# Kernel tuning notes

Hardware: AMD Instinct MI355X
Metric: run time of the kernel (lower is better)

The kernel has to match this reference:

```python
import jax, jax.numpy as jnp
import numpy as np
import math
from jax import lax

B, L, D, P, V, K = 4, 2048, 512, 128, 8, 4


def _lin(x, w, b):
    # torch Linear: y = x @ W^T + b, W shape (out, in)
    return jnp.einsum('...i,oi->...o', x, w) + b


def _gelu(v):
    return jax.nn.gelu(v, approximate=False)


def _dwconv_causal(x_ncl, w, b):
    # depthwise causal conv: torch Conv1d(groups=D, padding=K-1) then [:, :, :L]
    y = lax.conv_general_dilated(x_ncl, w, (1,), [(K - 1, 0)],
                                 dimension_numbers=('NCH', 'OIH', 'NCH'),
                                 feature_group_count=D)
    return y + b[None, :, None]


def _ln(v, g, b):
    m = v.mean(-1, keepdims=True)
    var = v.var(-1, keepdims=True)
    return (v - m) / jnp.sqrt(var + 1e-5) * g + b


def setup_inputs() -> dict:
    key = jax.random.key(0)
    it = iter(jax.random.split(key, 64))
    def nrm(shape, s=0.02):
        return jax.random.normal(next(it), shape, dtype=jnp.float32) * s
    z = lambda *s: jnp.zeros(s, jnp.float32)
    return dict(
        x=nrm((B, L, D), 1.0),
        lc_w=nrm((D, 1, K)), lc_b=z(D),
        cg_w=nrm((D, 1, K)), cg_b=z(D),
        cp_w=nrm((D, D)), cp_b=z(D),
        tw_w=nrm((D, D)), tw_b=z(D),
        omega_scale=jnp.full((D,), 0.01, jnp.float32),
        pi0_w=nrm((D, D)), pi0_b=z(D),
        pi2_w=nrm((D, D)), pi2_b=z(D),
        m1v_w=nrm((D, D)), m1v_b=z(D),
        m1o_w=nrm((D, D)), m1o_b=z(D),
        mag_w=nrm((D, D)), mag_b=z(D),
        mag_scale=jnp.asarray(5.0, jnp.float32),
        qo_w=nrm((D, D)), qo_b=z(D),
        ke_w=nrm((P, D)), ke_b=z(P),
        ve_w=nrm((V, D)), ve_b=z(V),
        sk0_w=nrm((D, 2 * D)), sk0_b=z(D),
        sk2_w=nrm((P, D)), sk2_b=z(P),
        sg_w=nrm((1, D)), sg_b=z(1),
        kvo_w=nrm((D, V)), kvo_b=z(D),
        ln_g=jnp.ones(5 * D, jnp.float32), ln_b=z(5 * D),
        o1_w=nrm((2 * D, 5 * D)), o1_b=z(2 * D),
        o2_w=nrm((D, 2 * D)), o2_b=z(D),
    )


def reference(x, lc_w, lc_b, cg_w, cg_b, cp_w, cp_b, tw_w, tw_b, omega_scale,
              pi0_w, pi0_b, pi2_w, pi2_b, m1v_w, m1v_b, m1o_w, m1o_b,
              mag_w, mag_b, mag_scale, qo_w, qo_b, ke_w, ke_b, ve_w, ve_b,
              sk0_w, sk0_b, sk2_w, sk2_b, sg_w, sg_b, kvo_w, kvo_b,
              ln_g, ln_b, o1_w, o1_b, o2_w, o2_b):
    Bs, Ls, Ds = x.shape
    # local gated causal depthwise conv branch
    xc = jnp.transpose(x, (0, 2, 1))                          # (B, D, L)
    co = _dwconv_causal(xc, lc_w, lc_b)
    cg = jax.nn.sigmoid(_dwconv_causal(xc, cg_w, cg_b))
    conv_out = _lin(jnp.transpose(co * cg, (0, 2, 1)), cp_w, cp_b)
    # evolving phases
    omega_scaled = _lin(x, tw_w, tw_b) * jnp.abs(omega_scale)
    phi = _lin(_gelu(_lin(x, pi0_w, pi0_b)), pi2_w, pi2_b) + jnp.cumsum(omega_scaled, axis=1)
    cos_phi = jnp.cos(phi)
    sin_phi = jnp.sin(phi)
    # magnitude-weighted phase memory
    v1 = _lin(x, m1v_w, m1v_b)
    magnitude = jax.nn.sigmoid(_lin(x, mag_w, mag_b)) * jnp.abs(mag_scale)
    wv1 = magnitude * v1
    sqrt_mag = jnp.sqrt(jnp.cumsum(magnitude, axis=1) + 1e-8)
    mem1_cos = jnp.cumsum(wv1 * cos_phi, axis=1) / sqrt_mag
    mem1_sin = jnp.cumsum(wv1 * sin_phi, axis=1) / sqrt_mag
    phi_q = phi + _lin(x, qo_w, qo_b)
    pos_ret = (mem1_cos * jnp.cos(phi_q) + mem1_sin * jnp.sin(phi_q)) / math.sqrt(Ds)
    pos_out = _lin(pos_ret, m1o_w, m1o_b)
    # phase-keyed associative KV memory
    query_phase = jnp.tanh(_lin(x, ke_w, ke_b)) * math.pi    # (B, L, P)
    values = _lin(x, ve_w, ve_b)                              # (B, L, V)
    store_gate = jax.nn.sigmoid(_lin(x, sg_w, sg_b))          # (B, L, 1)
    positions = jnp.arange(1, Ls + 1, dtype=x.dtype).reshape(1, -1, 1)
    context_avg = jnp.cumsum(x, axis=1) / positions
    storage_phase = jnp.tanh(_lin(_gelu(_lin(jnp.concatenate([x, context_avg], -1), sk0_w, sk0_b)), sk2_w, sk2_b)) * math.pi
    gated_vals = values * store_gate                          # (B, L, V)
    kv_mem_cos = jnp.cumsum(jnp.cos(storage_phase)[..., None] * gated_vals[:, :, None, :], axis=1)
    kv_mem_sin = jnp.cumsum(jnp.sin(storage_phase)[..., None] * gated_vals[:, :, None, :], axis=1)
    gate_norm = jnp.sqrt(jnp.maximum(jnp.cumsum(store_gate, axis=1), 1.0))[..., None]  # (B, L, 1, 1)
    kv_mem_cos = kv_mem_cos / gate_norm
    kv_mem_sin = kv_mem_sin / gate_norm
    kv_retrieved = (jnp.cos(query_phase)[..., None] * kv_mem_cos +
                    jnp.sin(query_phase)[..., None] * kv_mem_sin).sum(axis=2) / math.sqrt(P)
    kv_out = _lin(kv_retrieved, kvo_w, kvo_b)
    # combine (dropout is identity in eval)
    combined = jnp.concatenate([conv_out, pos_out, kv_out, x * cos_phi, x * sin_phi], axis=-1)
    h = _ln(combined, ln_g, ln_b)
    h = _lin(_gelu(_lin(h, o1_w, o1_b)), o2_w, o2_b)
    return x + h
```

## Files before the change

kernel.cpp:

```cpp
#include <hip/hip_runtime.h>
#include <cstdint>

typedef unsigned short u16;
typedef short short8 __attribute__((ext_vector_type(8)));
typedef float floatx4 __attribute__((ext_vector_type(4)));

#define B_ 4
#define L_ 2048
#define D_ 512
#define P_ 128
#define V_ 8
#define BL (B_ * L_)
#define NC_ 128
#define CH_ 16
#define PI_F 3.14159265358979323846f

__device__ inline u16 f2b(float f) {
    unsigned u = __float_as_uint(f);
    unsigned r = u + 0x7FFFu + ((u >> 16) & 1u);
    return (u16)(r >> 16);
}
__device__ inline float b2f(u16 h) {
    return __uint_as_float(((unsigned)h) << 16);
}
__device__ inline float gelu_f(float v) {
    return 0.5f * v * (1.0f + erff(v * 0.70710678118654752f));
}
__device__ inline float sigm(float v) {
    return 1.0f / (1.0f + __expf(-v));
}
__device__ inline float tanh_fast(float v) {
    return 1.0f - 2.0f / (1.0f + __expf(2.0f * v));
}

__device__ inline void async16(const u16* g, u16* l) {
    __builtin_amdgcn_global_load_lds(
        (const __attribute__((address_space(1))) unsigned int*)g,
        (__attribute__((address_space(3))) unsigned int*)l, 16, 0, 0);
}

extern __shared__ u16 smem_dyn[];

enum { EPI_F32 = 0, EPI_BF16 = 1, EPI_GELU_BF16 = 2, EPI_RESID_F32 = 3,
       EPI_PASS1 = 4, EPI_ATOMIC = 5 };

template <int EPI>
__device__ __forceinline__ void gemm_body(
    const u16* __restrict__ A, int lda,
    const u16* __restrict__ W, int ldw,
    const float* __restrict__ bias,
    void* __restrict__ Cout, int ldc, int N, int K,
    const float* __restrict__ resid, int mt, int nt)
{
    const int tid  = threadIdx.x;
    const int lane = tid & 63;
    const int wid  = tid >> 6;
    const int wm   = wid & 1, wn = wid >> 1;
    const int l16  = lane & 15, quad = lane >> 4;

    floatx4 acc[4][4] = {};

    const u16* Ab = A + (size_t)(mt * 128) * lda;
    const u16* Wb = W + (size_t)(nt * 128) * ldw;

    const int srow = lane >> 2;
    const int scol = (lane & 3) * 8;
    const u16* ga0 = Ab + (size_t)(wid * 16 + srow) * lda + scol;
    const u16* ga1 = Ab + (size_t)(64 + wid * 16 + srow) * lda + scol;
    const u16* gb0 = Wb + (size_t)(wid * 16 + srow) * ldw + scol;
    const u16* gb1 = Wb + (size_t)(64 + wid * 16 + srow) * ldw + scol;

    const int lA0 = (wid * 16) * 32;
    const int lA1 = (64 + wid * 16) * 32;

    const int nsteps = K >> 5;

    auto stage = [&](int t, int s) {
        u16* base = smem_dyn + s * 8192;
        const int ko = t * 32;
        async16(ga0 + ko, base + lA0);
        async16(ga1 + ko, base + lA1);
        async16(gb0 + ko, base + 4096 + lA0);
        async16(gb1 + ko, base + 4096 + lA1);
    };

    stage(0, 0);
    if (nsteps > 1) stage(1, 1);

    int s = 0;
    for (int t = 0; t < nsteps; ++t) {
        if (t + 1 < nsteps) {
            asm volatile("s_waitcnt vmcnt(4)" ::: "memory");
        } else {
            asm volatile("s_waitcnt vmcnt(0)" ::: "memory");
        }
        __builtin_amdgcn_s_barrier();
        asm volatile("" ::: "memory");
        if (t + 2 < nsteps) {
            int s2 = s + 2; if (s2 >= 3) s2 -= 3;
            stage(t + 2, s2);
        }
        const u16* As = smem_dyn + s * 8192;
        const u16* Bs = As + 4096;
        short8 a[4], b[4];
#pragma unroll
        for (int i = 0; i < 4; i++)
            a[i] = *(const short8*)(&As[(wm * 64 + i * 16 + l16) * 32 + quad * 8]);
#pragma unroll
        for (int j = 0; j < 4; j++)
            b[j] = *(const short8*)(&Bs[(wn * 64 + j * 16 + l16) * 32 + quad * 8]);
        __builtin_amdgcn_s_setprio(1);
#pragma unroll
        for (int i = 0; i < 4; i++)
#pragma unroll
            for (int j = 0; j < 4; j++)
                acc[i][j] = __builtin_amdgcn_mfma_f32_16x16x32_bf16(a[i], b[j], acc[i][j], 0, 0, 0);
        __builtin_amdgcn_s_setprio(0);
        ++s; if (s >= 3) s -= 3;
    }

#pragma unroll
    for (int i = 0; i < 4; i++) {
#pragma unroll
        for (int j = 0; j < 4; j++) {
#pragma unroll
            for (int r = 0; r < 4; r++) {
                int grow = mt * 128 + wm * 64 + i * 16 + quad * 4 + r;
                int gcol = nt * 128 + wn * 64 + j * 16 + l16;
                if (gcol < N) {
                    float v = acc[i][j][r] + (bias ? bias[gcol] : 0.0f);
                    size_t off = (size_t)grow * ldc + gcol;
                    if (EPI == EPI_F32)            ((float*)Cout)[off] = v;
                    else if (EPI == EPI_BF16)      ((u16*)Cout)[off] = f2b(v);
                    else if (EPI == EPI_GELU_BF16) ((u16*)Cout)[off] = f2b(gelu_f(v));
                    else if (EPI == EPI_PASS1) {
                        float vv = (gcol >= 512 && gcol < 1024) ? gelu_f(v) : v;
                        ((u16*)Cout)[off] = f2b(vv);
                    }
                    else if (EPI == EPI_RESID_F32) ((float*)Cout)[off] = v + resid[off];
                    else                           atomicAdd(&((float*)Cout)[off], v);
                }
            }
        }
    }
}

template <int EPI>
__global__ __launch_bounds__(256)
void gemm256(const u16* __restrict__ A, int lda,
             const u16* __restrict__ W, int ldw,
             const float* __restrict__ bias,
             void* __restrict__ C, int ldc, int N, int K,
             const float* __restrict__ resid)
{
    int kz = blockIdx.z;
    gemm_body<EPI>(A + (size_t)kz * K, lda, W + (size_t)kz * K, ldw,
                   kz == 0 ? bias : nullptr, C, ldc, N, K, resid,
                   blockIdx.x, blockIdx.y);
}

__global__ __launch_bounds__(256)
void mega1(const u16* __restrict__ xcat, const u16* __restrict__ convg,
           const u16* __restrict__ wcat1, const float* __restrict__ bcat1,
           const u16* __restrict__ kesgw, const float* __restrict__ kesgb,
           const u16* __restrict__ cpw, const float* __restrict__ cp_b,
           u16* __restrict__ out1, float* __restrict__ kesgo, u16* __restrict__ combined)
{
    int y = blockIdx.y, mt = blockIdx.x;
    if (y < 20)
        gemm_body<EPI_PASS1>(xcat, 1024, wcat1, 512, bcat1, out1, 2560, 2560, 512, nullptr, mt, y);
    else if (y < 22)
        gemm_body<EPI_F32>(xcat, 1024, kesgw, 512, kesgb, kesgo, 144, 144, 512, nullptr, mt, y - 20);
    else
        gemm_body<EPI_BF16>(convg, 512, cpw, 512, cp_b, combined, 2560, 512, 512, nullptr, mt, y - 22);
}

__global__ __launch_bounds__(256)
void mega2(const u16* __restrict__ posret, const u16* __restrict__ xcat,
           const u16* __restrict__ m1ow, const float* __restrict__ m1o_b,
           const u16* __restrict__ sk0w, const float* __restrict__ sk0_b,
           u16* __restrict__ combined, u16* __restrict__ sk0g)
{
    int y = blockIdx.y, mt = blockIdx.x;
    if (y < 4)
        gemm_body<EPI_BF16>(posret, 512, m1ow, 512, m1o_b, combined + 512, 2560, 512, 512, nullptr, mt, y);
    else
        gemm_body<EPI_GELU_BF16>(xcat, 1024, sk0w, 1024, sk0_b, sk0g, 512, 512, 1024, nullptr, mt, y - 4);
}

__global__ __launch_bounds__(256)
void prep_weights(const float* tw, const float* pi0, const float* m1v, const float* mag, const float* qo,
                  const float* ke, const float* ve, const float* sg,
                  const float* pi2, const float* cp, const float* sk0, const float* sk2,
                  const float* m1o, const float* o1, const float* o2,
                  const float* tw_b, const float* pi0_b, const float* m1v_b, const float* mag_b, const float* qo_b,
                  const float* ke_b, const float* ve_b, const float* sg_b,
                  u16* wcat1, float* bcat1, u16* kesgw, float* kesgb,
                  u16* pi2w, u16* cpw, u16* sk0w, u16* sk2w, u16* m1ow, u16* o1w, u16* o2w)
{
    int idx = blockIdx.x * 256 + threadIdx.x;
    const int n0 = 2560 * 512;
    const int n1 = n0 + 256 * 512;
    const int n2 = n1 + 512 * 512;
    const int n3 = n2 + 512 * 512;
    const int n4 = n3 + 512 * 1024;
    const int n5 = n4 + 128 * 512;
    const int n6 = n5 + 512 * 512;
    const int n7 = n6 + 1024 * 2560;
    const int n8 = n7 + 512 * 1024;
    const int n9 = n8 + 2560;
    const int n10 = n9 + 256;
    if (idx < n0) {
        int r = idx >> 9, k = idx & 511;
        const float* s = (r < 512) ? tw : (r < 1024) ? pi0 : (r < 1536) ? m1v : (r < 2048) ? mag : qo;
        wcat1[idx] = f2b(s[(r & 511) * 512 + k]);
    } else if (idx < n1) {
        int i = idx - n0; int r = i >> 9, k = i & 511;
        float v;
        if (r < 128)      v = ke[r * 512 + k];
        else if (r < 136) v = ve[(r - 128) * 512 + k];
        else if (r == 136) v = sg[k];
        else               v = 0.0f;
        kesgw[i] = f2b(v);
    }
    else if (idx < n2) { int i = idx - n1; pi2w[i] = f2b(pi2[i]); }
    else if (idx < n3) { int i = idx - n2; cpw[i]  = f2b(cp[i]); }
    else if (idx < n4) { int i = idx - n3; sk0w[i] = f2b(sk0[i]); }
    else if (idx < n5) { int i = idx - n4; sk2w[i] = f2b(sk2[i]); }
    else if (idx < n6) { int i = idx - n5; m1ow[i] = f2b(m1o[i]); }
    else if (idx < n7) { int i = idx - n6; o1w[i]  = f2b(o1[i]); }
    else if (idx < n8) { int i = idx - n7; o2w[i]  = f2b(o2[i]); }
    else if (idx < n9) {
        int i = idx - n8;
        const float* s = (i < 512) ? tw_b : (i < 1024) ? pi0_b : (i < 1536) ? m1v_b : (i < 2048) ? mag_b : qo_b;
        bcat1[i] = s[i & 511];
    } else if (idx < n10) {
        int i = idx - n9;
        kesgb[i] = (i < 128) ? ke_b[i] : (i < 136) ? ve_b[i - 128] : (i == 136) ? sg_b[0] : 0.0f;
    }
}

__global__ __launch_bounds__(256)
void conv_gate(const float* __restrict__ x,
               const float* __restrict__ lcw, const float* __restrict__ lcb,
               const float* __restrict__ cgw, const float* __restrict__ cgb,
               u16* __restrict__ out, u16* __restrict__ xcat)
{
    int idx = blockIdx.x * 256 + threadIdx.x;
    int d = idx & 511; int bl = idx >> 9;
    int l = bl & (L_ - 1); int b = bl >> 11;
    float a0 = 0.f, a1 = 0.f, xv3 = 0.f;
#pragma unroll
    for (int k = 0; k < 4; k++) {
        int ls = l - 3 + k;
        if (ls >= 0) {
            float xv = x[((size_t)(b * L_ + ls)) * 512 + d];
            if (k == 3) xv3 = xv;
            a0 += xv * lcw[d * 4 + k];
            a1 += xv * cgw[d * 4 + k];
        }
    }
    a0 += lcb[d];
    a1 = sigm(a1 + cgb[d]);
    out[idx] = f2b(a0 * a1);
    xcat[(size_t)bl * 1024 + d] = f2b(xv3);
}

__device__ __forceinline__ void scan_a_body(
    int blk, const u16* __restrict__ out1, const float* __restrict__ x,
    const float* __restrict__ oscale, const float* __restrict__ msc,
    float* __restrict__ cs_o, float* __restrict__ cs_x, float* __restrict__ cs_m)
{
    int nc = blk & 15, dt = (blk >> 4) & 7, b = blk >> 7;
    int t = threadIdx.x; int dl = t & 63, lg = t >> 6;
    int d = dt * 64 + dl;
    float os = fabsf(oscale[d]);
    float ms = fabsf(msc[0]);
    float so = 0.f, sx = 0.f, sm = 0.f;
    int l0 = nc * 128 + lg * 32;
    for (int i = 0; i < 32; i++) {
        size_t r = (size_t)(b * L_ + l0 + i);
        so += b2f(out1[r * 2560 + d]) * os;
        sm += sigm(b2f(out1[r * 2560 + 1536 + d])) * ms;
        sx += x[r * 512 + d];
    }
    __shared__ float sh[3][4][64];
    sh[0][lg][dl] = so; sh[1][lg][dl] = sx; sh[2][lg][dl] = sm;
    __syncthreads();
    if (t < 64) {
        float a = 0.f, xx = 0.f, m = 0.f;
        for (int g = 0; g < 4; g++) { a += sh[0][g][t]; xx += sh[1][g][t]; m += sh[2][g][t]; }
        size_t o = ((size_t)(b * 16 + nc)) * 512 + dt * 64 + t;
        cs_o[o] = a; cs_x[o] = xx; cs_m[o] = m;
    }
}

__device__ __forceinline__ void gate_body(const float* __restrict__ kesgo,
                                          float* __restrict__ gni)
{
    int b = threadIdx.x >> 6; int lane = threadIdx.x & 63;
    float v[32]; float s = 0.f;
#pragma unroll
    for (int i = 0; i < 32; i++) {
        int l = lane * 32 + i;
        v[i] = sigm(kesgo[((size_t)(b * L_ + l)) * 144 + 136]);
        s += v[i];
    }
    float sc = s;
#pragma unroll
    for (int ofs = 1; ofs < 64; ofs <<= 1) {
        float t = __shfl_up(sc, ofs, 64);
        if (lane >= ofs) sc += t;
    }
    float run = sc - s;
#pragma unroll
    for (int i = 0; i < 32; i++) {
        run += v[i];
        gni[b * L_ + lane * 32 + i] = rsqrtf(fmaxf(run, 1.0f));
    }
}

__global__ __launch_bounds__(256)
void stage2(const u16* __restrict__ out1, const u16* __restrict__ pi2w,
            const float* __restrict__ pi2_b, u16* __restrict__ phib,
            const float* __restrict__ x, const float* __restrict__ oscale,
            const float* __restrict__ msc,
            float* __restrict__ cs_o, float* __restrict__ cs_x, float* __restrict__ cs_m,
            const float* __restrict__ kesgo, float* __restrict__ gni)
{
    int blk = blockIdx.x;
    if (blk < 256)
        gemm_body<EPI_BF16>(out1 + 512, 2560, pi2w, 512, pi2_b, phib, 512, 512, 512,
                            nullptr, blk & 63, blk >> 6);
    else if (blk < 768)
        scan_a_body(blk - 256, out1, x, oscale, msc, cs_o, cs_x, cs_m);
    else
        gate_body(kesgo, gni);
}

__global__ __launch_bounds__(256)
void scan_c(const u16* __restrict__ out1, const u16* __restrict__ phib,
            const float* __restrict__ oscale, const float* __restrict__ msc,
            const float* __restrict__ cs_o,
            float* __restrict__ phi, float* __restrict__ cs_wc, float* __restrict__ cs_ws)
{
    int blk = blockIdx.x;
    int nc = blk & 15, dt = (blk >> 4) & 7, b = blk >> 7;
    int t = threadIdx.x; int dl = t & 63, lg = t >> 6;
    int d = dt * 64 + dl;
    float os = fabsf(oscale[d]);
    float ms = fabsf(msc[0]);
    int l0 = nc * 128 + lg * 32;
    float so = 0.f;
    for (int i = 0; i < 32; i++) {
        size_t r = (size_t)(b * L_ + l0 + i);
        so += b2f(out1[r * 2560 + d]) * os;
    }
    __shared__ float sh[4][64];
    __shared__ float shw[2][4][64];
    sh[lg][dl] = so;
    __syncthreads();
    float pre = 0.f;
    for (int p = 0; p < nc; p++) pre += cs_o[((size_t)(b * 16 + p)) * 512 + d];
    for (int g = 0; g < lg; g++) pre += sh[g][dl];
    float cum = pre, swc = 0.f, sws = 0.f;
    for (int i = 0; i < 32; i++) {
        size_t r = (size_t)(b * L_ + l0 + i);
        cum += b2f(out1[r * 2560 + d]) * os;
        float ph = b2f(phib[r * 512 + d]) + cum;
        phi[r * 512 + d] = ph;
        float mg = sigm(b2f(out1[r * 2560 + 1536 + d])) * ms;
        float wv = mg * b2f(out1[r * 2560 + 1024 + d]);
        float s = __sinf(ph), c = __cosf(ph);
        swc += wv * c; sws += wv * s;
    }
    shw[0][lg][dl] = swc; shw[1][lg][dl] = sws;
    __syncthreads();
    if (t < 64) {
        float a = 0.f, bb = 0.f;
        for (int g = 0; g < 4; g++) { a += shw[0][g][t]; bb += shw[1][g][t]; }
        size_t o = ((size_t)(b * 16 + nc)) * 512 + dt * 64 + t;
        cs_wc[o] = a; cs_ws[o] = bb;
    }
}

__global__ __launch_bounds__(256)
void scan_e(const u16* __restrict__ out1, const float* __restrict__ phi,
            const float* __restrict__ x, const float* __restrict__ msc,
            const float* __restrict__ cs_m, const float* __restrict__ cs_x,
            const float* __restrict__ cs_wc, const float* __restrict__ cs_ws,
            u16* __restrict__ posret, u16* __restrict__ xcat, u16* __restrict__ combined)
{
    int blk = blockIdx.x;
    int nc = blk & 15, dt = (blk >> 4) & 7, b = blk >> 7;
    int t = threadIdx.x; int dl = t & 63, lg = t >> 6;
    int d = dt * 64 + dl;
    float ms = fabsf(msc[0]);
    int l0 = nc * 128 + lg * 32;
    float sm = 0.f, swc = 0.f, sws = 0.f, sx = 0.f;
    for (int i = 0; i < 32; i++) {
        size_t r = (size_t)(b * L_ + l0 + i);
        float ph = phi[r * 512 + d];
        float mg = sigm(b2f(out1[r * 2560 + 1536 + d])) * ms;
        float wv = mg * b2f(out1[r * 2560 + 1024 + d]);
        float s = __sinf(ph), c = __cosf(ph);
        sm += mg; swc += wv * c; sws += wv * s; sx += x[r * 512 + d];
    }
    __shared__ float sh[4][4][64];
    sh[0][lg][dl] = sm; sh[1][lg][dl] = swc; sh[2][lg][dl] = sws; sh[3][lg][dl] = sx;
    __syncthreads();
    float cm = 0.f, cwc = 0.f, cws = 0.f, cx = 0.f;
    for (int p = 0; p < nc; p++) {
        size_t o = ((size_t)(b * 16 + p)) * 512 + d;
        cm += cs_m[o]; cwc += cs_wc[o]; cws += cs_ws[o]; cx += cs_x[o];
    }
    for (int g = 0; g < lg; g++) {
        cm += sh[0][g][dl]; cwc += sh[1][g][dl]; cws += sh[2][g][dl]; cx += sh[3][g][dl];
    }
    const float invsqD = 0.044194173824159216f;
    for (int i = 0; i < 32; i++) {
        int l = l0 + i;
        size_t r = (size_t)(b * L_ + l);
        float ph = phi[r * 512 + d];
        float mg = sigm(b2f(out1[r * 2560 + 1536 + d])) * ms;
        float wv = mg * b2f(out1[r * 2560 + 1024 + d]);
        float xv = x[r * 512 + d];
        float s = __sinf(ph), c = __cosf(ph);
        cm += mg; cwc += wv * c; cws += wv * s; cx += xv;
        float smag = sqrtf(cm + 1e-8f);
        float m1c = cwc / smag, m1s = cws / smag;
        float phq = ph + b2f(out1[r * 2560 + 2048 + d]);
        float sq = __sinf(phq), cq = __cosf(phq);
        float pr = (m1c * cq + m1s * sq) * invsqD;
        posret[r * 512 + d] = f2b(pr);
        xcat[r * 1024 + 512 + d] = f2b(cx / (float)(l + 1));
        combined[r * 2560 + 1536 + d] = f2b(xv * c);
        combined[r * 2560 + 2048 + d] = f2b(xv * s);
    }
}

__global__ __launch_bounds__(64)
void kv_chunk(const float* __restrict__ sppre, const float* __restrict__ kesgo,
              float* __restrict__ spc, float* __restrict__ sps,
              float* __restrict__ csum)
{
    int blk = blockIdx.x; int nc = blk & (NC_ - 1), b = blk >> 7;
    int t = threadIdx.x;
    float Sc[2][8] = {}, Ss[2][8] = {};
    for (int i = 0; i < CH_; i++) {
        size_t r = (size_t)(b * L_ + nc * CH_ + i);
        float sgate = sigm(kesgo[r * 144 + 136]);
        float g[8];
#pragma unroll
        for (int v = 0; v < 8; v++) g[v] = kesgo[r * 144 + 128 + v] * sgate;
#pragma unroll
        for (int j = 0; j < 2; j++) {
            int p = t + j * 64;
            float sp = tanh_fast(sppre[r * 128 + p]) * PI_F;
            float s = __sinf(sp), c = __cosf(sp);
            spc[r * 128 + p] = c; sps[r * 128 + p] = s;
#pragma unroll
            for (int v = 0; v < 8; v++) { Sc[j][v] += c * g[v]; Ss[j][v] += s * g[v]; }
        }
    }
    size_t base = (size_t)blk * 2048;
#pragma unroll
    for (int j = 0; j < 2; j++)
#pragma unroll
        for (int v = 0; v < 8; v++) {
            csum[base + (t + j * 64) * 8 + v]        = Sc[j][v];
            csum[base + 1024 + (t + j * 64) * 8 + v] = Ss[j][v];
        }
}

__global__ __launch_bounds__(256)
void kv_scan(const float* __restrict__ cin, float* __restrict__ cex)
{
    int t = blockIdx.x * 256 + threadIdx.x;
    int pv = t & 1023; int cs = (t >> 10) & 1; int b = t >> 11;
    float run = 0.f;
    for (int nc = 0; nc < NC_; nc++) {
        size_t o = ((size_t)(b * NC_ + nc)) * 2048 + cs * 1024 + pv;
        cex[o] = run; run += cin[o];
    }
}

__global__ __launch_bounds__(64)
void kv_retrieve(const float* __restrict__ spc, const float* __restrict__ sps,
                 const float* __restrict__ kesgo,
                 const float* __restrict__ gni, const float* __restrict__ cex,
                 const float* __restrict__ kvo_w, const float* __restrict__ kvo_b,
                 u16* __restrict__ combined)
{
    int blk = blockIdx.x; int nc = blk & (NC_ - 1), b = blk >> 7;
    int t = threadIdx.x;
    const int nb = t * 8;
    float wr[8][8], br[8];
#pragma unroll
    for (int n = 0; n < 8; n++) {
        *(float4*)&wr[n][0] = *(const float4*)&kvo_w[(nb + n) * 8];
        *(float4*)&wr[n][4] = *(const float4*)&kvo_w[(nb + n) * 8 + 4];
        br[n] = kvo_b[nb + n];
    }
    float Sc[2][8], Ss[2][8];
    size_t base = (size_t)blk * 2048;
#pragma unroll
    for (int j = 0; j < 2; j++)
#pragma unroll
        for (int v = 0; v < 8; v++) {
            Sc[j][v] = cex[base + (t + j * 64) * 8 + v];
            Ss[j][v] = cex[base + 1024 + (t + j * 64) * 8 + v];
        }
    for (int i = 0; i < CH_; i++) {
        size_t r = (size_t)(b * L_ + nc * CH_ + i);
        float sgate = sigm(kesgo[r * 144 + 136]);
        float g[8];
#pragma unroll
        for (int v = 0; v < 8; v++) g[v] = kesgo[r * 144 + 128 + v] * sgate;
        float part[8];
#pragma unroll
        for (int v = 0; v < 8; v++) part[v] = 0.f;
#pragma unroll
        for (int j = 0; j < 2; j++) {
            int p = t + j * 64;
            float c = spc[r * 128 + p], s = sps[r * 128 + p];
#pragma unroll
            for (int v = 0; v < 8; v++) { Sc[j][v] += c * g[v]; Ss[j][v] += s * g[v]; }
            float qp = tanh_fast(kesgo[r * 144 + p]) * PI_F;
            float sq = __sinf(qp), cq = __cosf(qp);
#pragma unroll
            for (int v = 0; v < 8; v++) part[v] += cq * Sc[j][v] + sq * Ss[j][v];
        }
#pragma unroll
        for (int ofs = 1; ofs < 64; ofs <<= 1)
#pragma unroll
            for (int v = 0; v < 8; v++) part[v] += __shfl_xor(part[v], ofs, 64);
        float scale = gni[r] * 0.08838834764831845f;
        float pv[8];
#pragma unroll
        for (int v = 0; v < 8; v++) pv[v] = part[v] * scale;
        u16 outv[8];
#pragma unroll
        for (int n = 0; n < 8; n++) {
            float a = br[n];
#pragma unroll
            for (int v = 0; v < 8; v++) a += pv[v] * wr[n][v];
            outv[n] = f2b(a);
        }
        *(uint4*)&combined[r * 2560 + 1024 + nb] = *(const uint4*)outv;
    }
}

__global__ __launch_bounds__(320)
void ln_rows(u16* __restrict__ combined, const float* __restrict__ g, const float* __restrict__ bb)
{
    size_t m = blockIdx.x; int t = threadIdx.x;
    u16 vv[8];
    *(uint4*)vv = *(const uint4*)&combined[m * 2560 + t * 8];
    float f[8]; float s = 0.f, s2 = 0.f;
#pragma unroll
    for (int k = 0; k < 8; k++) { f[k] = b2f(vv[k]); s += f[k]; s2 += f[k] * f[k]; }
#pragma unroll
    for (int ofs = 1; ofs < 64; ofs <<= 1) {
        s  += __shfl_xor(s, ofs, 64);
        s2 += __shfl_xor(s2, ofs, 64);
    }
    __shared__ float shs[5], shs2[5];
    int wv = t >> 6;
    if ((t & 63) == 0) { shs[wv] = s; shs2[wv] = s2; }
    __syncthreads();
    float S = 0.f, S2 = 0.f;
#pragma unroll
    for (int i = 0; i < 5; i++) { S += shs[i]; S2 += shs2[i]; }
    float mean = S * (1.0f / 2560.0f);
    float var  = S2 * (1.0f / 2560.0f) - mean * mean;
    float rstd = rsqrtf(var + 1e-5f);
#pragma unroll
    for (int k = 0; k < 8; k++) {
        int c = t * 8 + k;
        vv[k] = f2b((f[k] - mean) * rstd * g[c] + bb[c]);
    }
    *(uint4*)&combined[m * 2560 + t * 8] = *(const uint4*)vv;
}

extern "C" void kernel_launch(void* const* d_in, const int* in_sizes, int n_in,
                              void* d_out, int out_size, void* d_ws, size_t ws_size,
                              hipStream_t stream)
{
    const float* x     = (const float*)d_in[0];
    const float* lc_w  = (const float*)d_in[1];
    const float* lc_b  = (const float*)d_in[2];
    const float* cg_w  = (const float*)d_in[3];
    const float* cg_b  = (const float*)d_in[4];
    const float* cp_w  = (const float*)d_in[5];
    const float* cp_b  = (const float*)d_in[6];
    const float* tw_w  = (const float*)d_in[7];
    const float* tw_b  = (const float*)d_in[8];
    const float* omega_scale = (const float*)d_in[9];
    const float* pi0_w = (const float*)d_in[10];
    const float* pi0_b = (const float*)d_in[11];
    const float* pi2_w = (const float*)d_in[12];
    const float* pi2_b = (const float*)d_in[13];
    const float* m1v_w = (const float*)d_in[14];
    const float* m1v_b = (const float*)d_in[15];
    const float* m1o_w = (const float*)d_in[16];
    const float* m1o_b = (const float*)d_in[17];
    const float* mag_w = (const float*)d_in[18];
    const float* mag_b = (const float*)d_in[19];
    const float* mag_scale = (const float*)d_in[20];
    const float* qo_w  = (const float*)d_in[21];
    const float* qo_b  = (const float*)d_in[22];
    const float* ke_w  = (const float*)d_in[23];
    const float* ke_b  = (const float*)d_in[24];
    const float* ve_w  = (const float*)d_in[25];
    const float* ve_b  = (const float*)d_in[26];
    const float* sk0_w = (const float*)d_in[27];
    const float* sk0_b = (const float*)d_in[28];
    const float* sk2_w = (const float*)d_in[29];
    const float* sk2_b = (const float*)d_in[30];
    const float* sg_w  = (const float*)d_in[31];
    const float* sg_b  = (const float*)d_in[32];
    const float* kvo_w = (const float*)d_in[33];
    const float* kvo_b = (const float*)d_in[34];
    const float* ln_g  = (const float*)d_in[35];
    const float* ln_b  = (const float*)d_in[36];
    const float* o1_w  = (const float*)d_in[37];
    const float* o1_b  = (const float*)d_in[38];
    const float* o2_w  = (const float*)d_in[39];
    const float* o2_b  = (const float*)d_in[40];
    float* out = (float*)d_out;

    char* base = (char*)d_ws;
    size_t off = 0;
    auto alloc = [&](size_t bytes) -> void* {
        void* p = base + off;
        off += (bytes + 255) & ~(size_t)255;
        return p;
    };

    u16*   wcat1  = (u16*)  alloc((size_t)2560 * 512 * 2);
    float* bcat1  = (float*)alloc(2560 * 4);
    u16*   kesgw  = (u16*)  alloc((size_t)256 * 512 * 2);
    float* kesgb  = (float*)alloc(256 * 4);
    u16*   pi2w   = (u16*)  alloc((size_t)512 * 512 * 2);
    u16*   cpw    = (u16*)  alloc((size_t)512 * 512 * 2);
    u16*   sk0w   = (u16*)  alloc((size_t)512 * 1024 * 2);
    u16*   sk2w   = (u16*)  alloc((size_t)128 * 512 * 2);
    u16*   m1ow   = (u16*)  alloc((size_t)512 * 512 * 2);
    u16*   o1w    = (u16*)  alloc((size_t)1024 * 2560 * 2);
    u16*   o2w    = (u16*)  alloc((size_t)512 * 1024 * 2);
    u16*   xcat   = (u16*)  alloc((size_t)BL * 1024 * 2);
    u16*   out1   = (u16*)  alloc((size_t)BL * 2560 * 2);
    u16*   phib   = (u16*)  alloc((size_t)BL * 512 * 2);
    float* phi    = (float*)alloc((size_t)BL * 512 * 4);
    float* kesgo  = (float*)alloc((size_t)BL * 144 * 4);
    u16*   convg  = (u16*)  alloc((size_t)BL * 512 * 2);
    float* sppre  = (float*)alloc((size_t)BL * 128 * 4);
    u16*   combined = (u16*)alloc((size_t)BL * 2560 * 2);
    float* cs_o   = (float*)alloc((size_t)4 * 16 * 512 * 4);
    float* cs_x   = (float*)alloc((size_t)4 * 16 * 512 * 4);
    float* cs_m   = (float*)alloc((size_t)4 * 16 * 512 * 4);
    float* cs_wc  = (float*)alloc((size_t)4 * 16 * 512 * 4);
    float* cs_ws  = (float*)alloc((size_t)4 * 16 * 512 * 4);
    float* gni    = (float*)alloc((size_t)BL * 4);
    u16*   posret = convg;
    u16*   sk0g   = out1;
    float* spc    = phi;
    float* sps    = phi + (size_t)BL * 128;
    float* kvcs   = (float*)phib;
    float* kvex   = (float*)phib + (size_t)B_ * NC_ * 2048;
    u16*   o1g    = xcat;
    (void)ws_size; (void)in_sizes; (void)n_in; (void)out_size;

    const size_t SMEM = 49152;

    prep_weights<<<23307, 256, 0, stream>>>(
        tw_w, pi0_w, m1v_w, mag_w, qo_w, ke_w, ve_w, sg_w,
        pi2_w, cp_w, sk0_w, sk2_w, m1o_w, o1_w, o2_w,
        tw_b, pi0_b, m1v_b, mag_b, qo_b, ke_b, ve_b, sg_b,
        wcat1, bcat1, kesgw, kesgb, pi2w, cpw, sk0w, sk2w, m1ow, o1w, o2w);
    conv_gate<<<16384, 256, 0, stream>>>(x, lc_w, lc_b, cg_w, cg_b, convg, xcat);
    mega1<<<dim3(64, 26), 256, SMEM, stream>>>(xcat, convg, wcat1, bcat1,
                                               kesgw, kesgb, cpw, cp_b,
                                               out1, kesgo, combined);
    stage2<<<769, 256, SMEM, stream>>>(out1, pi2w, pi2_b, phib,
                                       x, omega_scale, mag_scale,
                                       cs_o, cs_x, cs_m, kesgo, gni);
    scan_c<<<512, 256, 0, stream>>>(out1, phib, omega_scale, mag_scale, cs_o,
                                    phi, cs_wc, cs_ws);
    scan_e<<<512, 256, 0, stream>>>(out1, phi, x, mag_scale, cs_m, cs_x, cs_wc, cs_ws,
                                    posret, xcat, combined);
    mega2<<<dim3(64, 8), 256, SMEM, stream>>>(posret, xcat, m1ow, m1o_b,
                                              sk0w, sk0_b, combined, sk0g);
    hipMemsetAsync(sppre, 0, (size_t)BL * 128 * 4, stream);
    gemm256<EPI_ATOMIC><<<dim3(64, 1, 4), 256, SMEM, stream>>>(sk0g, 512, sk2w, 512, sk2_b,
                                                               sppre, 128, 128, 128, nullptr);
    kv_chunk<<<4 * NC_, 64, 0, stream>>>(sppre, kesgo, spc, sps, kvcs);
    kv_scan<<<32, 256, 0, stream>>>(kvcs, kvex);
    kv_retrieve<<<4 * NC_, 64, 0, stream>>>(spc, sps, kesgo, gni, kvex, kvo_w, kvo_b, combined);
    ln_rows<<<8192, 320, 0, stream>>>(combined, ln_g, ln_b);
    gemm256<EPI_GELU_BF16><<<dim3(64, 8), 256, SMEM, stream>>>(combined, 2560, o1w, 2560, o1_b,
                                                               o1g, 1024, 1024, 2560, nullptr);
    gemm256<EPI_RESID_F32><<<dim3(64, 4), 256, SMEM, stream>>>(o1g, 1024, o2w, 1024, o2_b,
                                                               out, 512, 512, 1024, x);
}
```

Baseline: 557.4 us.

## Swizzle GEMM LDS layout and register-double-buffer fragments with deeper prefetch

The GEMM body now applies an XOR swizzle to the 16-byte column chunk used for both the async global-to-LDS stores and the fragment reads, to reduce LDS bank conflicts. The main loop is restructured to prefetch three stages up front and to ping-pong between two register fragment sets. Fragments for the next step are read from LDS while the MFMAs for the current step issue, hiding LDS latency behind matrix math. The cost is more VGPRs for the second fragment set, which may lower occupancy, plus more intricate wait and barrier accounting that is easy to get wrong.

```diff
diff --git a/kernel.cpp b/kernel.cpp
--- a/kernel.cpp
+++ b/kernel.cpp
@@ -57,6 +57,7 @@
     const int wid  = tid >> 6;
     const int wm   = wid & 1, wn = wid >> 1;
     const int l16  = lane & 15, quad = lane >> 4;
+    const int rswz = (l16 >> 1) & 3;
 
     floatx4 acc[4][4] = {};
 
@@ -64,7 +65,7 @@
     const u16* Wb = W + (size_t)(nt * 128) * ldw;
 
     const int srow = lane >> 2;
-    const int scol = (lane & 3) * 8;
+    const int scol = ((lane & 3) ^ ((srow >> 1) & 3)) * 8;
     const u16* ga0 = Ab + (size_t)(wid * 16 + srow) * lda + scol;
     const u16* ga1 = Ab + (size_t)(64 + wid * 16 + srow) * lda + scol;
     const u16* gb0 = Wb + (size_t)(wid * 16 + srow) * ldw + scol;
@@ -84,31 +85,18 @@
         async16(gb1 + ko, base + 4096 + lA1);
     };
 
-    stage(0, 0);
-    if (nsteps > 1) stage(1, 1);
-
-    int s = 0;
-    for (int t = 0; t < nsteps; ++t) {
-        if (t + 1 < nsteps) {
-            asm volatile("s_waitcnt vmcnt(4)" ::: "memory");
-        } else {
-            asm volatile("s_waitcnt vmcnt(0)" ::: "memory");
-        }
-        __builtin_amdgcn_s_barrier();
-        asm volatile("" ::: "memory");
-        if (t + 2 < nsteps) {
-            int s2 = s + 2; if (s2 >= 3) s2 -= 3;
-            stage(t + 2, s2);
-        }
-        const u16* As = smem_dyn + s * 8192;
+    auto readfrag = [&](int slot, short8 (&a)[4], short8 (&b)[4]) {
+        const u16* As = smem_dyn + slot * 8192;
         const u16* Bs = As + 4096;
-        short8 a[4], b[4];
 #pragma unroll
         for (int i = 0; i < 4; i++)
-            a[i] = *(const short8*)(&As[(wm * 64 + i * 16 + l16) * 32 + quad * 8]);
+            a[i] = *(const short8*)(&As[(wm * 64 + i * 16 + l16) * 32 + (quad ^ rswz) * 8]);
 #pragma unroll
         for (int j = 0; j < 4; j++)
-            b[j] = *(const short8*)(&Bs[(wn * 64 + j * 16 + l16) * 32 + quad * 8]);
+            b[j] = *(const short8*)(&Bs[(wn * 64 + j * 16 + l16) * 32 + (quad ^ rswz) * 8]);
+    };
+
+    auto mfma16 = [&](short8 (&a)[4], short8 (&b)[4]) {
         __builtin_amdgcn_s_setprio(1);
 #pragma unroll
         for (int i = 0; i < 4; i++)
@@ -116,7 +104,38 @@
             for (int j = 0; j < 4; j++)
                 acc[i][j] = __builtin_amdgcn_mfma_f32_16x16x32_bf16(a[i], b[j], acc[i][j], 0, 0, 0);
         __builtin_amdgcn_s_setprio(0);
-        ++s; if (s >= 3) s -= 3;
+    };
+
+    stage(0, 0);
+    if (nsteps > 1) stage(1, 1);
+    if (nsteps > 2) stage(2, 2);
+    if (nsteps > 2)      asm volatile("s_waitcnt vmcnt(8)" ::: "memory");
+    else if (nsteps > 1) asm volatile("s_waitcnt vmcnt(4)" ::: "memory");
+    else                 asm volatile("s_waitcnt vmcnt(0)" ::: "memory");
+    __builtin_amdgcn_s_barrier();
+    asm volatile("" ::: "memory");
+
+    short8 aE[4], bE[4], aO[4], bO[4];
+    readfrag(0, aE, bE);
+
+    for (int t = 0; t < nsteps; t += 2) {
+        asm volatile("s_waitcnt lgkmcnt(0)" ::: "memory");
+        if (t + 2 < nsteps)      asm volatile("s_waitcnt vmcnt(4)" ::: "memory");
+        else if (t + 1 < nsteps) asm volatile("s_waitcnt vmcnt(0)" ::: "memory");
+        __builtin_amdgcn_s_barrier();
+        asm volatile("" ::: "memory");
+        if (t + 3 < nsteps) stage(t + 3, t % 3);
+        if (t + 1 < nsteps) readfrag((t + 1) % 3, aO, bO);
+        mfma16(aE, bE);
+        const int t1 = t + 1;
+        asm volatile("s_waitcnt lgkmcnt(0)" ::: "memory");
+        if (t1 + 2 < nsteps)      asm volatile("s_waitcnt vmcnt(4)" ::: "memory");
+        else if (t1 + 1 < nsteps) asm volatile("s_waitcnt vmcnt(0)" ::: "memory");
+        __builtin_amdgcn_s_barrier();
+        asm volatile("" ::: "memory");
+        if (t1 + 3 < nsteps) stage(t1 + 3, t1 % 3);
+        if (t1 + 1 < nsteps) readfrag((t1 + 1) % 3, aE, bE);
+        mfma16(aO, bO);
     }
 
 #pragma unroll
```

Result: no change. 560.4 us (+0.5%).
